# Performance work log

Hardware: AMD Instinct MI355X
Metric: run time of the kernel (lower is better)

The kernel has to match this reference:

```python
import jax, jax.numpy as jnp
import numpy as np

B, T, D = 4096, 64, 256       # expressions, max tokens per expression, encoding dim
N_SYM, N_OCC = 20000, 131072  # symbols, symbol occurrences


def setup_inputs() -> dict:
    key = jax.random.key(0)
    k1, k2, k3, k4, k5 = jax.random.split(key, 5)
    # unique flattened occurrence positions -> deterministic scatter
    rng = np.random.default_rng(0)
    flat_pos = rng.permutation(B * T)[:N_OCC].astype(np.int64)
    return {
        "expressions_encodings": jax.random.normal(k1, (B, T, D), dtype=jnp.float32),
        "symbols_encodings": jax.random.normal(k2, (N_SYM, D), dtype=jnp.float32),
        "Wf": jax.random.normal(k3, (D, 2 * D), dtype=jnp.float32) * 0.05,
        "bf": jnp.zeros((D,), dtype=jnp.float32),
        "Wa": jax.random.normal(k4, (D, 2 * D), dtype=jnp.float32) * 0.05,
        "ba": jnp.zeros((D,), dtype=jnp.float32),
        "expr_idx": jnp.asarray(flat_pos // T),
        "token_idx": jnp.asarray(flat_pos % T),
        "symbol_idx": jax.random.randint(k5, (N_OCC,), 0, N_SYM, dtype=jnp.int64),
    }


def reference(expressions_encodings, symbols_encodings, Wf, bf, Wa, ba,
              expr_idx, token_idx, symbol_idx):
    b, t, d = expressions_encodings.shape
    flat = expressions_encodings.reshape(b * t, d)            # [B*T, D]
    occ_pos = t * expr_idx + token_idx                        # [N_OCC]
    prev = flat[occ_pos]                                      # gather: [N_OCC, D]
    upd = symbols_encodings[symbol_idx]                       # gather: [N_OCC, D]
    concat = jnp.concatenate([prev, upd], axis=-1)            # [N_OCC, 2D]
    forget = jax.nn.sigmoid(concat @ Wf.T + bf)               # forget gate
    add = jax.nn.sigmoid(concat @ Wa.T + ba)                  # add gate
    new_occ = forget * prev + add * upd                       # gated update
    out = flat.at[occ_pos].set(new_occ)                       # scatter back
    return out.reshape(b, t, d)
```

## Files before the change

kernel.cpp:

```cpp
#include <hip/hip_runtime.h>

typedef __attribute__((ext_vector_type(8))) short short8;
typedef __attribute__((ext_vector_type(4))) short short4v;
typedef __attribute__((ext_vector_type(4))) float floatx4;

__device__ __forceinline__ unsigned short f2bf(float f) {
    unsigned int u = __float_as_uint(f);
    u += 0x7FFFu + ((u >> 16) & 1u);
    return (unsigned short)(u >> 16);
}
__device__ __forceinline__ float bf2f(unsigned short s) {
    return __uint_as_float(((unsigned int)s) << 16);
}
__device__ __forceinline__ float sigmoidf(float x) {
    return 1.f / (1.f + __expf(-x));
}

__global__ __launch_bounds__(256)
void convert_w_kernel(const float* __restrict__ Wf,
                      const float* __restrict__ Wa,
                      short* __restrict__ wswz)
{
    int id = blockIdx.x * 256 + threadIdx.x;
    int slot = id & 63;
    int ks   = (id >> 6) & 15;
    int g    = id >> 10;
    int l15  = slot & 15, lk = slot >> 4;
    const float* base = (g < 16) ? (Wf + (long)(g * 16 + l15) * 512)
                                 : (Wa + (long)((g - 16) * 16 + l15) * 512);
    const float* src = base + ks * 32 + lk * 8;
    floatx4 w0 = *(const floatx4*)src;
    floatx4 w1 = *(const floatx4*)(src + 4);
    short8 o;
    o[0] = (short)f2bf(w0[0]); o[1] = (short)f2bf(w0[1]);
    o[2] = (short)f2bf(w0[2]); o[3] = (short)f2bf(w0[3]);
    o[4] = (short)f2bf(w1[0]); o[5] = (short)f2bf(w1[1]);
    o[6] = (short)f2bf(w1[2]); o[7] = (short)f2bf(w1[3]);
    *(short8*)(wswz + (long)id * 8) = o;
}

__global__ __launch_bounds__(256)
void mark_kernel(const int* __restrict__ ei, const int* __restrict__ ti,
                 unsigned char* __restrict__ flags, int n)
{
    int i = blockIdx.x * 256 + threadIdx.x;
    if (i < n) flags[64 * ei[i] + ti[i]] = 1;
}

__global__ __launch_bounds__(256)
void copy_rest_kernel(const float* __restrict__ flat,
                      const unsigned char* __restrict__ flags,
                      float* __restrict__ out, int nrows)
{
    const int lane = threadIdx.x & 63;
    const int w0   = (blockIdx.x * 256 + threadIdx.x) >> 6;
    const int nw   = (gridDim.x * 256) >> 6;
    for (int row = w0; row < nrows; row += nw) {
        if (flags[row]) continue;
        const floatx4* s = (const floatx4*)(flat + (long)row * 256);
        floatx4*       o = (floatx4*)(out + (long)row * 256);
        o[lane] = s[lane];
    }
}

__global__ __launch_bounds__(512, 4)
void gate_gemm_kernel(const float* __restrict__ flat,
                      const float* __restrict__ syms,
                      const float* __restrict__ bfb,
                      const float* __restrict__ bab,
                      const int* __restrict__ expr_idx,
                      const int* __restrict__ token_idx,
                      const int* __restrict__ sym_idx,
                      const short* __restrict__ wswz,
                      float* __restrict__ out)
{
    __shared__ __align__(16) short A_lds[64][520];
    __shared__ int rowbuf[64];
    __shared__ int symbuf[64];

    const int tid  = threadIdx.x;
    const int occ0 = blockIdx.x * 64;

    if (tid < 64) {
        int occ = occ0 + tid;
        rowbuf[tid] = 64 * expr_idx[occ] + token_idx[occ];
        symbuf[tid] = sym_idx[occ];
    }
    __syncthreads();

    {
        const int srow = tid >> 3;
        const int se   = tid & 7;
        const float* prow = flat + (long)rowbuf[srow] * 256;
        const float* urow = syms + (long)symbuf[srow] * 256;
        #pragma unroll
        for (int it = 0; it < 8; ++it) {
            const int k = (se + it * 8) * 4;
            floatx4 v = *(const floatx4*)(prow + k);
            short4v sv;
            sv[0] = (short)f2bf(v[0]); sv[1] = (short)f2bf(v[1]);
            sv[2] = (short)f2bf(v[2]); sv[3] = (short)f2bf(v[3]);
            *(short4v*)&A_lds[srow][k] = sv;
        }
        #pragma unroll
        for (int it = 0; it < 8; ++it) {
            const int k = (se + it * 8) * 4;
            floatx4 v = *(const floatx4*)(urow + k);
            short4v sv;
            sv[0] = (short)f2bf(v[0]); sv[1] = (short)f2bf(v[1]);
            sv[2] = (short)f2bf(v[2]); sv[3] = (short)f2bf(v[3]);
            *(short4v*)&A_lds[srow][256 + k] = sv;
        }
    }
    __syncthreads();

    const int lane = tid & 63;
    const int wv   = tid >> 6;
    const int l15  = lane & 15;
    const int lk   = lane >> 4;

    floatx4 acc[4][4];
    #pragma unroll
    for (int mi = 0; mi < 4; ++mi)
        #pragma unroll
        for (int c = 0; c < 4; ++c)
            acc[mi][c] = (floatx4){0.f, 0.f, 0.f, 0.f};

    const short8* wsv = (const short8*)wswz;

    #pragma unroll
    for (int ks = 0; ks < 16; ++ks) {
        short8 cb[4];
        #pragma unroll
        for (int mi = 0; mi < 4; ++mi)
            cb[mi] = *(const short8*)&A_lds[mi * 16 + l15][ks * 32 + lk * 8];

        #pragma unroll
        for (int c = 0; c < 4; ++c) {
            const int g = (c < 2) ? (wv * 2 + c) : (16 + wv * 2 + (c - 2));
            short8 wf = wsv[(g * 16 + ks) * 64 + lane];
            #pragma unroll
            for (int mi = 0; mi < 4; ++mi)
                acc[mi][c] = __builtin_amdgcn_mfma_f32_16x16x32_bf16(
                    wf, cb[mi], acc[mi][c], 0, 0, 0);
        }
    }

    #pragma unroll
    for (int c = 0; c < 2; ++c) {
        const int d0 = wv * 32 + c * 16 + lk * 4;
        const floatx4 bfv = *(const floatx4*)(bfb + d0);
        const floatx4 bav = *(const floatx4*)(bab + d0);
        #pragma unroll
        for (int mi = 0; mi < 4; ++mi) {
            const int m = mi * 16 + l15;
            short4v pv = *(const short4v*)&A_lds[m][d0];
            short4v uv = *(const short4v*)&A_lds[m][256 + d0];
            floatx4 res;
            #pragma unroll
            for (int j = 0; j < 4; ++j) {
                float fg = sigmoidf(acc[mi][c][j]     + bfv[j]);
                float ag = sigmoidf(acc[mi][c + 2][j] + bav[j]);
                res[j] = fg * bf2f((unsigned short)pv[j])
                       + ag * bf2f((unsigned short)uv[j]);
            }
            *(floatx4*)(out + (long)rowbuf[m] * 256 + d0) = res;
        }
    }
}

extern "C" void kernel_launch(void* const* d_in, const int* in_sizes, int n_in,
                              void* d_out, int out_size, void* d_ws, size_t ws_size,
                              hipStream_t stream) {
    const float* flat = (const float*)d_in[0];
    const float* syms = (const float*)d_in[1];
    const float* Wf   = (const float*)d_in[2];
    const float* bf   = (const float*)d_in[3];
    const float* Wa   = (const float*)d_in[4];
    const float* ba   = (const float*)d_in[5];
    const int* ei     = (const int*)d_in[6];
    const int* ti     = (const int*)d_in[7];
    const int* si     = (const int*)d_in[8];
    float* out        = (float*)d_out;

    short* wswz          = (short*)d_ws;
    unsigned char* flags = (unsigned char*)d_ws + 512 * 1024;

    const int n_occ = in_sizes[6];
    const int nrows = out_size / 256;

    hipMemsetAsync(flags, 0, nrows, stream);
    mark_kernel<<<(n_occ + 255) / 256, 256, 0, stream>>>(ei, ti, flags, n_occ);

    convert_w_kernel<<<128, 256, 0, stream>>>(Wf, Wa, wswz);

    gate_gemm_kernel<<<n_occ / 64, 512, 0, stream>>>(flat, syms, bf, ba,
                                                     ei, ti, si, wswz, out);

    copy_rest_kernel<<<2048, 256, 0, stream>>>(flat, flags, out, nrows);
}
```

Baseline: 241.5 us.

## Restructure gate kernel gathers, swizzle LDS, stage coalesced output through shared memory

```diff
diff --git a/kernel.cpp b/kernel.cpp
--- a/kernel.cpp
+++ b/kernel.cpp
@@ -40,6 +40,12 @@
 }
 
 __global__ __launch_bounds__(256)
+void zero_flags_kernel(unsigned int* __restrict__ flags)
+{
+    flags[blockIdx.x * 256 + threadIdx.x] = 0u;
+}
+
+__global__ __launch_bounds__(256)
 void mark_kernel(const int* __restrict__ ei, const int* __restrict__ ti,
                  unsigned char* __restrict__ flags, int n)
 {
@@ -64,60 +70,57 @@
 }
 
 __global__ __launch_bounds__(512, 4)
-void gate_gemm_kernel(const float* __restrict__ flat,
-                      const float* __restrict__ syms,
-                      const float* __restrict__ bfb,
-                      const float* __restrict__ bab,
-                      const int* __restrict__ expr_idx,
-                      const int* __restrict__ token_idx,
-                      const int* __restrict__ sym_idx,
-                      const short* __restrict__ wswz,
-                      float* __restrict__ out)
-{
-    __shared__ __align__(16) short A_lds[64][520];
-    __shared__ int rowbuf[64];
-    __shared__ int symbuf[64];
+void gate_kernel(const float* __restrict__ flat,
+                 const float* __restrict__ syms,
+                 const float* __restrict__ bfb,
+                 const float* __restrict__ bab,
+                 const int* __restrict__ ei,
+                 const int* __restrict__ ti,
+                 const int* __restrict__ si,
+                 const short* __restrict__ wswz,
+                 float* __restrict__ out)
+{
+    __shared__ __align__(16) short A_lds[64 * 512];
 
     const int tid  = threadIdx.x;
+    const int lane = tid & 63;
+    const int w    = tid >> 6;
     const int occ0 = blockIdx.x * 64;
 
-    if (tid < 64) {
-        int occ = occ0 + tid;
-        rowbuf[tid] = 64 * expr_idx[occ] + token_idx[occ];
-        symbuf[tid] = sym_idx[occ];
+    int rowi[8];
+    {
+        int symi[8];
+        #pragma unroll
+        for (int i = 0; i < 8; ++i) {
+            const int occ = occ0 + w * 8 + i;
+            rowi[i] = 64 * ei[occ] + ti[occ];
+            symi[i] = si[occ];
+        }
+        floatx4 va[8], vb[8];
+        #pragma unroll
+        for (int i = 0; i < 8; ++i) {
+            const float* base = (lane < 32)
+                ? (flat + (long)rowi[i] * 256 + lane * 8)
+                : (syms + (long)symi[i] * 256 + (lane - 32) * 8);
+            va[i] = *(const floatx4*)base;
+            vb[i] = *(const floatx4*)(base + 4);
+        }
+        #pragma unroll
+        for (int i = 0; i < 8; ++i) {
+            short8 o;
+            o[0] = (short)f2bf(va[i][0]); o[1] = (short)f2bf(va[i][1]);
+            o[2] = (short)f2bf(va[i][2]); o[3] = (short)f2bf(va[i][3]);
+            o[4] = (short)f2bf(vb[i][0]); o[5] = (short)f2bf(vb[i][1]);
+            o[6] = (short)f2bf(vb[i][2]); o[7] = (short)f2bf(vb[i][3]);
+            const int r = w * 8 + i;
+            *(short8*)&A_lds[r * 512 + ((lane ^ (r & 7)) << 3)] = o;
+        }
     }
     __syncthreads();
 
-    {
-        const int srow = tid >> 3;
-        const int se   = tid & 7;
-        const float* prow = flat + (long)rowbuf[srow] * 256;
-        const float* urow = syms + (long)symbuf[srow] * 256;
-        #pragma unroll
-        for (int it = 0; it < 8; ++it) {
-            const int k = (se + it * 8) * 4;
-            floatx4 v = *(const floatx4*)(prow + k);
-            short4v sv;
-            sv[0] = (short)f2bf(v[0]); sv[1] = (short)f2bf(v[1]);
-            sv[2] = (short)f2bf(v[2]); sv[3] = (short)f2bf(v[3]);
-            *(short4v*)&A_lds[srow][k] = sv;
-        }
-        #pragma unroll
-        for (int it = 0; it < 8; ++it) {
-            const int k = (se + it * 8) * 4;
-            floatx4 v = *(const floatx4*)(urow + k);
-            short4v sv;
-            sv[0] = (short)f2bf(v[0]); sv[1] = (short)f2bf(v[1]);
-            sv[2] = (short)f2bf(v[2]); sv[3] = (short)f2bf(v[3]);
-            *(short4v*)&A_lds[srow][256 + k] = sv;
-        }
-    }
-    __syncthreads();
-
-    const int lane = tid & 63;
-    const int wv   = tid >> 6;
-    const int l15  = lane & 15;
-    const int lk   = lane >> 4;
+    const int l15 = lane & 15;
+    const int lk  = lane >> 4;
+    const short8* wsv = (const short8*)wswz;
 
     floatx4 acc[4][4];
     #pragma unroll
@@ -126,46 +129,65 @@
         for (int c = 0; c < 4; ++c)
             acc[mi][c] = (floatx4){0.f, 0.f, 0.f, 0.f};
 
-    const short8* wsv = (const short8*)wswz;
-
     #pragma unroll
     for (int ks = 0; ks < 16; ++ks) {
         short8 cb[4];
         #pragma unroll
-        for (int mi = 0; mi < 4; ++mi)
-            cb[mi] = *(const short8*)&A_lds[mi * 16 + l15][ks * 32 + lk * 8];
-
+        for (int mi = 0; mi < 4; ++mi) {
+            const int m  = mi * 16 + l15;
+            const int ch = (ks * 4 + lk) ^ (m & 7);
+            cb[mi] = *(const short8*)&A_lds[m * 512 + (ch << 3)];
+        }
         #pragma unroll
         for (int c = 0; c < 4; ++c) {
-            const int g = (c < 2) ? (wv * 2 + c) : (16 + wv * 2 + (c - 2));
-            short8 wf = wsv[(g * 16 + ks) * 64 + lane];
+            const int g = (c < 2) ? (w * 2 + c) : (16 + w * 2 + (c - 2));
+            const short8 wf = wsv[(g * 16 + ks) * 64 + lane];
             #pragma unroll
             for (int mi = 0; mi < 4; ++mi)
                 acc[mi][c] = __builtin_amdgcn_mfma_f32_16x16x32_bf16(
                     wf, cb[mi], acc[mi][c], 0, 0, 0);
         }
     }
+    __syncthreads();
 
     #pragma unroll
     for (int c = 0; c < 2; ++c) {
-        const int d0 = wv * 32 + c * 16 + lk * 4;
+        const int d0 = w * 32 + c * 16 + lk * 4;
         const floatx4 bfv = *(const floatx4*)(bfb + d0);
         const floatx4 bav = *(const floatx4*)(bab + d0);
         #pragma unroll
         for (int mi = 0; mi < 4; ++mi) {
-            const int m = mi * 16 + l15;
-            short4v pv = *(const short4v*)&A_lds[m][d0];
-            short4v uv = *(const short4v*)&A_lds[m][256 + d0];
-            floatx4 res;
+            const int m  = mi * 16 + l15;
+            const int sw = m & 7;
+            const int cp = (d0 >> 3) ^ sw;
+            const int cu = (32 + (d0 >> 3)) ^ sw;
+            const int sub = d0 & 7;
+            short4v pv = *(const short4v*)&A_lds[m * 512 + (cp << 3) + sub];
+            short4v uv = *(const short4v*)&A_lds[m * 512 + (cu << 3) + sub];
+            short4v o;
             #pragma unroll
             for (int j = 0; j < 4; ++j) {
                 float fg = sigmoidf(acc[mi][c][j]     + bfv[j]);
                 float ag = sigmoidf(acc[mi][c + 2][j] + bav[j]);
-                res[j] = fg * bf2f((unsigned short)pv[j])
-                       + ag * bf2f((unsigned short)uv[j]);
+                o[j] = (short)f2bf(fg * bf2f((unsigned short)pv[j])
+                                 + ag * bf2f((unsigned short)uv[j]));
             }
-            *(floatx4*)(out + (long)rowbuf[m] * 256 + d0) = res;
-        }
+            *(short4v*)&A_lds[m * 512 + (cp << 3) + sub] = o;
+        }
+    }
+    __syncthreads();
+
+    #pragma unroll
+    for (int i = 0; i < 8; ++i) {
+        const int r = w * 8 + i;
+        short4v s = *(const short4v*)
+            &A_lds[r * 512 + (((lane >> 1) ^ (r & 7)) << 3) + (lane & 1) * 4];
+        floatx4 o4;
+        o4[0] = bf2f((unsigned short)s[0]);
+        o4[1] = bf2f((unsigned short)s[1]);
+        o4[2] = bf2f((unsigned short)s[2]);
+        o4[3] = bf2f((unsigned short)s[3]);
+        *(floatx4*)(out + (long)rowi[i] * 256 + lane * 4) = o4;
     }
 }
 
@@ -189,13 +211,12 @@
     const int n_occ = in_sizes[6];
     const int nrows = out_size / 256;
 
-    hipMemsetAsync(flags, 0, nrows, stream);
+    zero_flags_kernel<<<nrows / 1024, 256, 0, stream>>>((unsigned int*)flags);
     mark_kernel<<<(n_occ + 255) / 256, 256, 0, stream>>>(ei, ti, flags, n_occ);
-
     convert_w_kernel<<<128, 256, 0, stream>>>(Wf, Wa, wswz);
 
-    gate_gemm_kernel<<<n_occ / 64, 512, 0, stream>>>(flat, syms, bf, ba,
-                                                     ei, ti, si, wswz, out);
+    gate_kernel<<<n_occ / 64, 512, 0, stream>>>(flat, syms, bf, ba,
+                                                ei, ti, si, wswz, out);
 
     copy_rest_kernel<<<2048, 256, 0, stream>>>(flat, flags, out, nrows);
 }
```

Result: faster. 231.8 us (-4.0%).
